# Kernel tuning notes

Hardware: AMD Instinct MI355X
Metric: run time of the kernel (lower is better)

## Reference

```python
import jax, jax.numpy as jnp
import numpy as np

T_STEPS, N_GRID = 730, 8000
NEARZERO = 1e-5
# parameter bounds, order: tt ddf alpha beta stor retip fscn scx flz stot cgw resmax k1 k2 k3 k4 k5 k6
_BOUNDS = [(-3,5),(0,20),(0,1),(0,1),(0,5),(0,50),(0,1),(0,1),(0.005,0.995),(1,2000),(0,20),(1,300),(0,1),(1,5),(0,1),(0,1),(0,1),(0,1)]
_LO = jnp.array([b[0] for b in _BOUNDS], dtype=jnp.float32)
_HI = jnp.array([b[1] for b in _BOUNDS], dtype=jnp.float32)


def setup_inputs() -> dict:
    key = jax.random.key(0)
    kx, kp = jax.random.split(key)
    x = jax.random.uniform(kx, (T_STEPS, N_GRID, 3), dtype=jnp.float32)
    # scale forcings to physical ranges: prcp in [0,10) mm/d, tmean in [-2,6) C, pet in [0,5) mm/d
    x = x * jnp.array([10.0, 8.0, 5.0], dtype=jnp.float32) + jnp.array([0.0, -2.0, 0.0], dtype=jnp.float32)
    parameters = jax.random.normal(kp, (T_STEPS, N_GRID, 18), dtype=jnp.float32)
    return {"x": x, "parameters": parameters}


def _prms_forward(x, parameters):
    # static params: sigmoid of NN output at static_idx = warm_up - 1 = -1, scaled to bounds
    p = jax.nn.sigmoid(parameters[-1, :, :18])            # [N, 18]
    p = _LO + p * (_HI - _LO)
    p = p[:, :, None]                                      # [N, 18, 1]  (nmul = 1)
    (tt, ddf, alpha, beta, stor, retip, fscn, scx, flz, stot,
     cgw, resmax, k1, k2, k3, k4, k5, k6) = [p[:, i] for i in range(18)]
    scn = fscn * scx
    remx = (1.0 - flz) * stot
    smax = flz * stot

    Pm = x[:, :, 0:1]    # precipitation [T, N, 1]
    Tm = x[:, :, 1:2]    # mean temperature
    PETm = x[:, :, 2:3]  # potential ET

    n_grid = x.shape[1]
    s0 = jnp.full((n_grid, 1), 0.001, dtype=jnp.float32)
    init = (s0, s0, s0, s0, s0, s0, s0)  # snow, XIN, RSTOR, RECHR, SMAV, RES, GW

    def step(state, inp):
        snow, xin, rstor, rechr, smav, res, gw = state
        PRECIP, temp, Ep = inp
        # snow partition and melt (delta_t = 1)
        is_snow = (temp <= tt).astype(jnp.float32)
        flux_ps = PRECIP * is_snow
        flux_pr = PRECIP * (1.0 - is_snow)
        snow = snow + flux_ps
        flux_m = jnp.maximum(ddf * (temp - tt), 0.0)
        flux_m = jnp.minimum(flux_m, snow)
        snow = jnp.maximum(snow - flux_m, NEARZERO)
        # interception
        flux_pim = flux_pr * (1.0 - beta)
        flux_psm = flux_pr * beta
        flux_pby = flux_psm * (1.0 - alpha)
        flux_pin = flux_psm * alpha
        xin = xin + flux_pin
        flux_ptf = jnp.maximum(xin - stor, 0.0)
        xin = jnp.maximum(xin - flux_ptf, NEARZERO)
        flux_ein = jnp.minimum(Ep * beta, xin)
        xin = jnp.maximum(xin - flux_ein, NEARZERO)
        # impervious reservoir
        flux_mim = flux_m * (1.0 - beta)
        flux_msm = flux_m * beta
        rstor = rstor + flux_mim + flux_pim
        flux_sas = jnp.maximum(rstor - retip, 0.0)
        rstor = jnp.maximum(rstor - flux_sas, NEARZERO)
        flux_eim = jnp.minimum((1.0 - beta) * Ep, rstor)
        rstor = jnp.maximum(rstor - flux_eim, NEARZERO)
        # surface runoff / infiltration to recharge zone
        sro_lin = jnp.clip(scn + (scx - scn) * (rechr / remx), 0.0, 1.0)
        inflow = flux_msm + flux_ptf + flux_pby
        flux_sro = sro_lin * inflow
        flux_inf = inflow - flux_sro
        rechr = rechr + flux_inf
        flux_pc = jnp.maximum(rechr - remx, 0.0)
        rechr = rechr - flux_pc
        evap_max_a = jnp.maximum(rechr / remx * (Ep - flux_ein - flux_eim), 0.0)
        flux_ea = jnp.minimum(evap_max_a, rechr)
        rechr = jnp.maximum(rechr - flux_ea, NEARZERO)
        # lower soil moisture zone
        smav = smav + flux_pc
        flux_excs = jnp.maximum(smav - smax, 0.0)
        smav = smav - flux_excs
        transp = jnp.where(rechr < (Ep - flux_ein - flux_eim),
                           jnp.maximum(smav / smax * (Ep - flux_ein - flux_eim - flux_ea), 0.0),
                           jnp.zeros_like(smav))
        transp = jnp.minimum(transp, smav)
        smav = jnp.maximum(smav - transp, NEARZERO)
        # seepage and subsurface reservoir
        flux_sep = jnp.minimum(cgw, flux_excs)
        flux_qres = jnp.maximum(flux_excs - flux_sep, 0.0)
        res = res + flux_qres
        flux_gad = k1 * (res / resmax) ** k2
        flux_gad = jnp.minimum(flux_gad, res)
        res = jnp.maximum(res - flux_gad, NEARZERO)
        flux_ras = k3 * res + k4 * res * res
        flux_ras = jnp.minimum(flux_ras, res)
        res = jnp.maximum(res - flux_ras, NEARZERO)
        # groundwater
        gw = gw + flux_gad + flux_sep
        flux_bas = k5 * gw
        gw = jnp.maximum(gw - flux_bas, NEARZERO)
        flux_snk = k6 * gw
        gw = jnp.maximum(gw - flux_snk, NEARZERO)
        q = flux_sas + flux_sro + flux_bas + flux_ras
        return (snow, xin, rstor, rechr, smav, res, gw), q

    _, Q = jax.lax.scan(step, init, (Pm, Tm, PETm))
    return Q  # [T, N, 1]


def reference(x, parameters):
    return _prms_forward(x, parameters)
```

## Files before the change

### kernel.cpp

```cpp
#include <hip/hip_runtime.h>
#include <math.h>

#define T_STEPS 730
#define N_GRID  8000
#define NEARZERO 1e-5f

__constant__ float c_lo[18] = {-3.f, 0.f, 0.f, 0.f, 0.f, 0.f, 0.f, 0.f, 0.005f, 1.f,    0.f, 1.f,   0.f, 1.f, 0.f, 0.f, 0.f, 0.f};
__constant__ float c_hi[18] = { 5.f, 20.f, 1.f, 1.f, 5.f, 50.f, 1.f, 1.f, 0.995f, 2000.f, 20.f, 300.f, 1.f, 5.f, 1.f, 1.f, 1.f, 1.f};

#define EXP2F(v) __builtin_amdgcn_exp2f(v)
#define LOG2F(v) __builtin_amdgcn_logf(v)

__global__ __launch_bounds__(64, 1) void prms_kernel(
    const float* __restrict__ x,
    const float* __restrict__ params,
    float* __restrict__ out)
{
    const int i = blockIdx.x * 64 + threadIdx.x;

    const float* pp = params + ((size_t)(T_STEPS - 1) * N_GRID + (size_t)i) * 18;
    float pr[18];
#pragma unroll
    for (int j = 0; j < 18; ++j) {
        float s = 1.0f / (1.0f + expf(-pp[j]));
        pr[j] = c_lo[j] + s * (c_hi[j] - c_lo[j]);
    }
    const float tt = pr[0],  ddf = pr[1],  alpha = pr[2], beta = pr[3];
    const float stor = pr[4], retip = pr[5], fscn = pr[6], scx = pr[7];
    const float flz = pr[8],  stot = pr[9],  cgw = pr[10], resmax = pr[11];
    const float k1 = pr[12],  k2 = pr[13],  k3 = pr[14],  k4 = pr[15];
    const float k5 = pr[16],  k6 = pr[17];

    const float scn      = fscn * scx;
    const float remx     = (1.0f - flz) * stot;
    const float smax     = flz * stot;
    const float inv_remx = 1.0f / remx;
    const float inv_smax = 1.0f / smax;
    const float ombeta   = 1.0f - beta;
    const float omalpha  = 1.0f - alpha;
    const float omscn    = 1.0f - scn;
    const float omk3     = 1.0f - k3;
    const float omk56    = (1.0f - k5) * (1.0f - k6);
    const float dscn     = (scx - scn) * inv_remx;
    const float pow_c2   = fmaf(k2, LOG2F(1.0f / resmax), LOG2F(k1));

    float snow = 0.001f, xin = 0.001f, rstor = 0.001f, rechr = 0.001f;
    float smav = 0.001f, res = 0.001f, gw = 0.001f;

    constexpr int CH = 10;
    float3 buf[CH];
#pragma unroll
    for (int u = 0; u < CH; ++u) {
        const float* q = x + ((size_t)u * N_GRID + (size_t)i) * 3;
        buf[u] = make_float3(q[0], q[1], q[2]);
    }

    for (int t0 = 0; t0 < T_STEPS; t0 += CH) {
        float3 nbuf[CH];
        const int tn = t0 + CH;
        if (tn < T_STEPS) {
#pragma unroll
            for (int u = 0; u < CH; ++u) {
                const float* q = x + ((size_t)(tn + u) * N_GRID + (size_t)i) * 3;
                nbuf[u] = make_float3(q[0], q[1], q[2]);
            }
        }

#pragma unroll
        for (int u = 0; u < CH; ++u) {
            const float PRECIP = buf[u].x;
            const float temp   = buf[u].y;
            const float Ep     = buf[u].z;

            const bool  snowy     = (temp <= tt);
            const float flux_ps   = snowy ? PRECIP : 0.0f;
            const float flux_pr   = PRECIP - flux_ps;
            const float m0        = fmaxf(ddf * (temp - tt), 0.0f);
            const float ps_m      = flux_ps - m0;
            const float flux_pim  = flux_pr * ombeta;
            const float flux_psm  = flux_pr * beta;
            const float flux_pby  = flux_psm * omalpha;
            const float flux_pin  = flux_psm * alpha;
            const float eb        = Ep * beta;
            const float eim_cap   = ombeta * Ep;
            const float pin_eb    = flux_pin - eb;
            const float stor_eb   = stor - eb;
            const float retip_eim = retip - eim_cap;

            const float snow1  = snow + flux_ps;
            const float flux_m = fminf(m0, snow1);
            snow = fmaxf(snow + ps_m, NEARZERO);

            const float xin1     = xin + flux_pin;
            const float flux_ptf = fmaxf(xin1 - stor, 0.0f);
            const float xin2     = fmaxf(fminf(xin1, stor), NEARZERO);
            const float flux_ein = fminf(eb, xin2);
            xin = fmaxf(fminf(xin + pin_eb, stor_eb), NEARZERO);

            const float flux_mim = flux_m * ombeta;
            const float rstor1   = rstor + (flux_mim + flux_pim);
            const float flux_sas = fmaxf(rstor1 - retip, 0.0f);
            const float rstor2   = fmaxf(fminf(rstor1, retip), NEARZERO);
            const float flux_eim = fminf(eim_cap, rstor2);
            rstor = fmaxf(fminf(rstor1 - eim_cap, retip_eim), NEARZERO);

            const float flux_msm = flux_m * beta;
            const float inflow   = flux_msm + (flux_ptf + flux_pby);
            const float tkeep    = fminf(fmaxf(fmaf(-dscn, rechr, omscn), 0.0f), 1.0f);
            const float flux_inf = inflow * tkeep;
            const float flux_sro = inflow - flux_inf;

            const float rechr1  = fmaf(inflow, tkeep, rechr);
            const float flux_pc = fmaxf(rechr1 - remx, 0.0f);
            const float rechr2  = fminf(rechr1, remx);
            const float ep_rem  = Ep - flux_ein - flux_eim;
            const float cfac    = inv_remx * ep_rem;
            const float emax    = rechr2 * cfac;
            const float flux_ea = fminf(emax, rechr2);
            rechr = fmaxf(rechr2 * (1.0f - cfac), NEARZERO);

            const float smav1     = smav + flux_pc;
            const float flux_excs = fmaxf(smav1 - smax, 0.0f);
            const float smav2     = fminf(smav1, smax);
            const float gfac      = inv_smax * (ep_rem - flux_ea);
            const float hkeep     = (rechr < ep_rem) ? (1.0f - gfac) : 1.0f;
            smav = fmaxf(smav2 * hkeep, NEARZERO);

            const float flux_sep  = fminf(cgw, flux_excs);
            const float flux_qres = fmaxf(flux_excs - cgw, 0.0f);
            const float res1      = res + flux_qres;
            const float gad0      = EXP2F(fmaf(k2, LOG2F(res1), pow_c2));
            const float flux_gad  = fminf(gad0, res1);
            const float res2      = fmaxf(res1 - gad0, NEARZERO);
            const float ras0      = fmaf(k4, res2, k3) * res2;
            const float flux_ras  = fminf(ras0, res2);
            res = fmaxf(res2 * fmaf(-k4, res2, omk3), NEARZERO);

            const float gw1      = gw + (flux_gad + flux_sep);
            const float flux_bas = k5 * gw1;
            gw = fmaxf(gw1 * omk56, NEARZERO);

            const float q = (flux_sas + flux_sro) + (flux_bas + flux_ras);
            out[(size_t)(t0 + u) * N_GRID + (size_t)i] = q;
        }

#pragma unroll
        for (int u = 0; u < CH; ++u) buf[u] = nbuf[u];
    }
}

extern "C" void kernel_launch(void* const* d_in, const int* in_sizes, int n_in,
                              void* d_out, int out_size, void* d_ws, size_t ws_size,
                              hipStream_t stream) {
    const float* x      = (const float*)d_in[0];
    const float* params = (const float*)d_in[1];
    float* out          = (float*)d_out;
    prms_kernel<<<dim3(N_GRID / 64), dim3(64), 0, stream>>>(x, params, out);
}
```

Baseline: 668.1 us.

## Split the per-cell scan into a two-wavefront producer/consumer pipeline through LDS

Each block now runs two wavefronts over the same 64 cells. Wave 0 runs the snow, interception and depression-storage stages and writes inflow, remaining PET and surface runoff into a double-buffered LDS array. Wave 1 consumes these one chunk later and runs the soil, subsurface and groundwater stages. The aim is to shorten the serial dependency chain each wave walks per time step, since the kernel has few threads and is latency-bound. The cost is a block barrier every chunk, LDS traffic, and a redundant duplicate forcing-load block in the producer.

```diff
diff --git a/kernel.cpp b/kernel.cpp
--- a/kernel.cpp
+++ b/kernel.cpp
@@ -11,12 +11,19 @@
 #define EXP2F(v) __builtin_amdgcn_exp2f(v)
 #define LOG2F(v) __builtin_amdgcn_logf(v)
 
-__global__ __launch_bounds__(64, 1) void prms_kernel(
+constexpr int CH  = 10;
+constexpr int NCH = T_STEPS / CH;
+
+__global__ __launch_bounds__(128, 1) void prms_kernel(
     const float* __restrict__ x,
     const float* __restrict__ params,
     float* __restrict__ out)
 {
-    const int i = blockIdx.x * 64 + threadIdx.x;
+    const int lane = threadIdx.x & 63;
+    const int wv   = threadIdx.x >> 6;
+    const int i    = blockIdx.x * 64 + lane;
+
+    __shared__ float4 hx[2][CH][64];
 
     const float* pp = params + ((size_t)(T_STEPS - 1) * N_GRID + (size_t)i) * 18;
     float pr[18];
@@ -25,127 +32,158 @@
         float s = 1.0f / (1.0f + expf(-pp[j]));
         pr[j] = c_lo[j] + s * (c_hi[j] - c_lo[j]);
     }
-    const float tt = pr[0],  ddf = pr[1],  alpha = pr[2], beta = pr[3];
-    const float stor = pr[4], retip = pr[5], fscn = pr[6], scx = pr[7];
-    const float flz = pr[8],  stot = pr[9],  cgw = pr[10], resmax = pr[11];
-    const float k1 = pr[12],  k2 = pr[13],  k3 = pr[14],  k4 = pr[15];
-    const float k5 = pr[16],  k6 = pr[17];
 
-    const float scn      = fscn * scx;
-    const float remx     = (1.0f - flz) * stot;
-    const float smax     = flz * stot;
-    const float inv_remx = 1.0f / remx;
-    const float inv_smax = 1.0f / smax;
-    const float ombeta   = 1.0f - beta;
-    const float omalpha  = 1.0f - alpha;
-    const float omscn    = 1.0f - scn;
-    const float omk3     = 1.0f - k3;
-    const float omk56    = (1.0f - k5) * (1.0f - k6);
-    const float dscn     = (scx - scn) * inv_remx;
-    const float pow_c2   = fmaf(k2, LOG2F(1.0f / resmax), LOG2F(k1));
+    if (wv == 0) {
+        const float tt = pr[0],  ddf = pr[1], alpha = pr[2], beta = pr[3];
+        const float stor = pr[4], retip = pr[5];
+        const float ombeta  = 1.0f - beta;
+        const float omalpha = 1.0f - alpha;
 
-    float snow = 0.001f, xin = 0.001f, rstor = 0.001f, rechr = 0.001f;
-    float smav = 0.001f, res = 0.001f, gw = 0.001f;
+        float snow = 0.001f, xin = 0.001f, rstor = 0.001f;
 
-    constexpr int CH = 10;
-    float3 buf[CH];
+        float3 buf[CH];
 #pragma unroll
-    for (int u = 0; u < CH; ++u) {
-        const float* q = x + ((size_t)u * N_GRID + (size_t)i) * 3;
-        buf[u] = make_float3(q[0], q[1], q[2]);
-    }
-
-    for (int t0 = 0; t0 < T_STEPS; t0 += CH) {
-        float3 nbuf[CH];
-        const int tn = t0 + CH;
-        if (tn < T_STEPS) {
-#pragma unroll
-            for (int u = 0; u < CH; ++u) {
-                const float* q = x + ((size_t)(tn + u) * N_GRID + (size_t)i) * 3;
-                nbuf[u] = make_float3(q[0], q[1], q[2]);
-            }
+        for (int u = 0; u < CH; ++u) {
+            const float* q = x + ((size_t)u * N_GRID + (size_t)i) * 3;
+            buf[u] = make_float3(q[0], q[1], q[2]);
         }
 
+        for (int c = 0; c <= NCH; ++c) {
+            if (c < NCH) {
+                float3 nbuf[CH];
+                if (c + 1 < NCH) {
 #pragma unroll
-        for (int u = 0; u < CH; ++u) {
-            const float PRECIP = buf[u].x;
-            const float temp   = buf[u].y;
-            const float Ep     = buf[u].z;
-
-            const bool  snowy     = (temp <= tt);
-            const float flux_ps   = snowy ? PRECIP : 0.0f;
-            const float flux_pr   = PRECIP - flux_ps;
-            const float m0        = fmaxf(ddf * (temp - tt), 0.0f);
-            const float ps_m      = flux_ps - m0;
-            const float flux_pim  = flux_pr * ombeta;
-            const float flux_psm  = flux_pr * beta;
-            const float flux_pby  = flux_psm * omalpha;
-            const float flux_pin  = flux_psm * alpha;
-            const float eb        = Ep * beta;
-            const float eim_cap   = ombeta * Ep;
-            const float pin_eb    = flux_pin - eb;
-            const float stor_eb   = stor - eb;
-            const float retip_eim = retip - eim_cap;
-
-            const float snow1  = snow + flux_ps;
-            const float flux_m = fminf(m0, snow1);
-            snow = fmaxf(snow + ps_m, NEARZERO);
-
-            const float xin1     = xin + flux_pin;
-            const float flux_ptf = fmaxf(xin1 - stor, 0.0f);
-            const float xin2     = fmaxf(fminf(xin1, stor), NEARZERO);
-            const float flux_ein = fminf(eb, xin2);
-            xin = fmaxf(fminf(xin + pin_eb, stor_eb), NEARZERO);
-
-            const float flux_mim = flux_m * ombeta;
-            const float rstor1   = rstor + (flux_mim + flux_pim);
-            const float flux_sas = fmaxf(rstor1 - retip, 0.0f);
-            const float rstor2   = fmaxf(fminf(rstor1, retip), NEARZERO);
-            const float flux_eim = fminf(eim_cap, rstor2);
-            rstor = fmaxf(fminf(rstor1 - eim_cap, retip_eim), NEARZERO);
-
-            const float flux_msm = flux_m * beta;
-            const float inflow   = flux_msm + (flux_ptf + flux_pby);
-            const float tkeep    = fminf(fmaxf(fmaf(-dscn, rechr, omscn), 0.0f), 1.0f);
-            const float flux_inf = inflow * tkeep;
-            const float flux_sro = inflow - flux_inf;
-
-            const float rechr1  = fmaf(inflow, tkeep, rechr);
-            const float flux_pc = fmaxf(rechr1 - remx, 0.0f);
-            const float rechr2  = fminf(rechr1, remx);
-            const float ep_rem  = Ep - flux_ein - flux_eim;
-            const float cfac    = inv_remx * ep_rem;
-            const float emax    = rechr2 * cfac;
-            const float flux_ea = fminf(emax, rechr2);
-            rechr = fmaxf(rechr2 * (1.0f - cfac), NEARZERO);
-
-            const float smav1     = smav + flux_pc;
-            const float flux_excs = fmaxf(smav1 - smax, 0.0f);
-            const float smav2     = fminf(smav1, smax);
-            const float gfac      = inv_smax * (ep_rem - flux_ea);
-            const float hkeep     = (rechr < ep_rem) ? (1.0f - gfac) : 1.0f;
-            smav = fmaxf(smav2 * hkeep, NEARZERO);
-
-            const float flux_sep  = fminf(cgw, flux_excs);
-            const float flux_qres = fmaxf(flux_excs - cgw, 0.0f);
-            const float res1      = res + flux_qres;
-            const float gad0      = EXP2F(fmaf(k2, LOG2F(res1), pow_c2));
-            const float flux_gad  = fminf(gad0, res1);
-            const float res2      = fmaxf(res1 - gad0, NEARZERO);
-            const float ras0      = fmaf(k4, res2, k3) * res2;
-            const float flux_ras  = fminf(ras0, res2);
-            res = fmaxf(res2 * fmaf(-k4, res2, omk3), NEARZERO);
-
-            const float gw1      = gw + (flux_gad + flux_sep);
-            const float flux_bas = k5 * gw1;
-            gw = fmaxf(gw1 * omk56, NEARZERO);
-
-            const float q = (flux_sas + flux_sro) + (flux_bas + flux_ras);
-            out[(size_t)(t0 + u) * N_GRID + (size_t)i] = q;
-        }
+                    for (int u = 0; u < CH; ++u) {
+                        const float* q = x + ((size_t)((c + 1) * CH + u) * N_GRID + (size_t)i) * 3;
+                        nbuf[u] = make_float3(q[0], q[1], q[2]);
+                    }
+                }
 
 #pragma unroll
-        for (int u = 0; u < CH; ++u) buf[u] = nbuf[u];
+                for (int u = 0; u < CH; ++u) {
+                    const float PRECIP = buf[u].x;
+                    const float temp   = buf[u].y;
+                    const float Ep     = buf[u].z;
+
+                    const bool  snowy     = (temp <= tt);
+                    const float flux_ps   = snowy ? PRECIP : 0.0f;
+                    const float flux_pr   = PRECIP - flux_ps;
+                    const float m0        = fmaxf(ddf * (temp - tt), 0.0f);
+                    const float ps_m      = flux_ps - m0;
+                    const float flux_pim  = flux_pr * ombeta;
+                    const float flux_psm  = flux_pr * beta;
+                    const float flux_pby  = flux_psm * omalpha;
+                    const float flux_pin  = flux_psm * alpha;
+                    const float eb        = Ep * beta;
+                    const float eim_cap   = ombeta * Ep;
+                    const float pin_eb    = flux_pin - eb;
+                    const float stor_eb   = stor - eb;
+                    const float retip_eim = retip - eim_cap;
+
+                    const float snow1  = snow + flux_ps;
+                    const float flux_m = fminf(m0, snow1);
+                    snow = fmaxf(snow + ps_m, NEARZERO);
+
+                    const float xin1     = xin + flux_pin;
+                    const float flux_ptf = fmaxf(xin1 - stor, 0.0f);
+                    const float xin2     = fmaxf(fminf(xin1, stor), NEARZERO);
+                    const float flux_ein = fminf(eb, xin2);
+                    xin = fmaxf(fminf(xin + pin_eb, stor_eb), NEARZERO);
+
+                    const float flux_mim = flux_m * ombeta;
+                    const float rstor1   = rstor + (flux_mim + flux_pim);
+                    const float flux_sas = fmaxf(rstor1 - retip, 0.0f);
+                    const float rstor2   = fmaxf(fminf(rstor1, retip), NEARZERO);
+                    const float flux_eim = fminf(eim_cap, rstor2);
+                    rstor = fmaxf(fminf(rstor1 - eim_cap, retip_eim), NEARZERO);
+
+                    const float flux_msm = flux_m * beta;
+                    const float inflow   = flux_msm + (flux_ptf + flux_pby);
+                    const float ep_rem   = Ep - flux_ein - flux_eim;
+                    hx[c & 1][u][lane] = make_float4(inflow, ep_rem, flux_sas, 0.0f);
+                }
+
+                if (c + 1 < NCH) {
+                    float3 nbuf[CH];
+#pragma unroll
+                    for (int u = 0; u < CH; ++u) {
+                        const float* q = x + ((size_t)((c + 1) * CH + u) * N_GRID + (size_t)i) * 3;
+                        nbuf[u] = make_float3(q[0], q[1], q[2]);
+                    }
+#pragma unroll
+                    for (int u = 0; u < CH; ++u) buf[u] = nbuf[u];
+                }
+            }
+            __syncthreads();
+        }
+    } else {
+        const float fscn = pr[6], scx = pr[7], flz = pr[8], stot = pr[9];
+        const float cgw = pr[10], resmax = pr[11];
+        const float k1 = pr[12], k2 = pr[13], k3 = pr[14], k4 = pr[15];
+        const float k5 = pr[16], k6 = pr[17];
+
+        const float scn      = fscn * scx;
+        const float remx     = (1.0f - flz) * stot;
+        const float smax     = flz * stot;
+        const float inv_remx = 1.0f / remx;
+        const float inv_smax = 1.0f / smax;
+        const float omscn    = 1.0f - scn;
+        const float omk3     = 1.0f - k3;
+        const float omk56    = (1.0f - k5) * (1.0f - k6);
+        const float dscn     = (scx - scn) * inv_remx;
+        const float pow_c2   = fmaf(k2, LOG2F(1.0f / resmax), LOG2F(k1));
+
+        float rechr = 0.001f, smav = 0.001f, res = 0.001f, gw = 0.001f;
+
+        for (int c = 0; c <= NCH; ++c) {
+            if (c > 0) {
+                const int cc = c - 1;
+#pragma unroll
+                for (int u = 0; u < CH; ++u) {
+                    const float4 h = hx[cc & 1][u][lane];
+                    const float inflow   = h.x;
+                    const float ep_rem   = h.y;
+                    const float flux_sas = h.z;
+
+                    const float tkeep    = fminf(fmaxf(fmaf(-dscn, rechr, omscn), 0.0f), 1.0f);
+                    const float flux_inf = inflow * tkeep;
+                    const float flux_sro = inflow - flux_inf;
+
+                    const float rechr1  = fmaf(inflow, tkeep, rechr);
+                    const float flux_pc = fmaxf(rechr1 - remx, 0.0f);
+                    const float rechr2  = fminf(rechr1, remx);
+                    const float cfac    = inv_remx * ep_rem;
+                    const float emax    = rechr2 * cfac;
+                    const float flux_ea = fminf(emax, rechr2);
+                    rechr = fmaxf(rechr2 * (1.0f - cfac), NEARZERO);
+
+                    const float smav1     = smav + flux_pc;
+                    const float flux_excs = fmaxf(smav1 - smax, 0.0f);
+                    const float smav2     = fminf(smav1, smax);
+                    const float gfac      = inv_smax * (ep_rem - flux_ea);
+                    const float hkeep     = (rechr < ep_rem) ? (1.0f - gfac) : 1.0f;
+                    smav = fmaxf(smav2 * hkeep, NEARZERO);
+
+                    const float flux_sep  = fminf(cgw, flux_excs);
+                    const float flux_qres = fmaxf(flux_excs - cgw, 0.0f);
+                    const float res1      = res + flux_qres;
+                    const float gad0      = EXP2F(fmaf(k2, LOG2F(res1), pow_c2));
+                    const float flux_gad  = fminf(gad0, res1);
+                    const float res2      = fmaxf(res1 - gad0, NEARZERO);
+                    const float ras0      = fmaf(k4, res2, k3) * res2;
+                    const float flux_ras  = fminf(ras0, res2);
+                    res = fmaxf(res2 * fmaf(-k4, res2, omk3), NEARZERO);
+
+                    const float gw1      = gw + (flux_gad + flux_sep);
+                    const float flux_bas = k5 * gw1;
+                    gw = fmaxf(gw1 * omk56, NEARZERO);
+
+                    const float q = (flux_sas + flux_sro) + (flux_bas + flux_ras);
+                    out[(size_t)(cc * CH + u) * N_GRID + (size_t)i] = q;
+                }
+            }
+            __syncthreads();
+        }
     }
 }
 
@@ -155,5 +193,5 @@
     const float* x      = (const float*)d_in[0];
     const float* params = (const float*)d_in[1];
     float* out          = (float*)d_out;
-    prms_kernel<<<dim3(N_GRID / 64), dim3(64), 0, stream>>>(x, params, out);
+    prms_kernel<<<dim3(N_GRID / 64), dim3(128), 0, stream>>>(x, params, out);
 }
```

Result: faster. 611.2 us (-8.5%).
